# Kernel optimization log

Hardware: AMD Instinct MI355X
Metric: run time of the kernel (lower is better)

Reference implementation:

```python
import jax, jax.numpy as jnp
import numpy as np

N_NODES = 18870
HIDDEN = 256
K = 20
HEAD_HIDDEN = 512
N_CLASSES = 3
N_GENES_OUT = 6640
B = 1024
FALLBACK_SCALE = 1e-3
LN_EPS = 1e-5


def setup_inputs() -> dict:
    key = jax.random.key(0)
    ks = jax.random.split(key, 8)
    node_idx = jax.random.randint(ks[0], (B,), 0, N_NODES)
    topk_neighbors = jax.random.randint(ks[1], (N_NODES, K), 0, N_NODES)
    node_emb = jax.random.normal(ks[2], (N_NODES, HIDDEN), dtype=jnp.float32)
    fallback_emb = jax.random.normal(ks[3], (HIDDEN,), dtype=jnp.float32) * 0.02
    w_attn = jax.random.normal(ks[4], (HIDDEN,), dtype=jnp.float32) * 0.02
    ln_gamma = jnp.ones((2 * HIDDEN,), dtype=jnp.float32)
    ln_beta = jnp.zeros((2 * HIDDEN,), dtype=jnp.float32)
    W1 = jax.random.normal(ks[5], (2 * HIDDEN, HEAD_HIDDEN), dtype=jnp.float32) * 0.02
    b1 = jnp.zeros((HEAD_HIDDEN,), dtype=jnp.float32)
    W2 = jax.random.normal(ks[6], (HEAD_HIDDEN, N_CLASSES * N_GENES_OUT), dtype=jnp.float32) * 0.02
    b2 = jnp.zeros((N_CLASSES * N_GENES_OUT,), dtype=jnp.float32)
    return dict(node_idx=node_idx, topk_neighbors=topk_neighbors, node_emb=node_emb,
                fallback_emb=fallback_emb, w_attn=w_attn, ln_gamma=ln_gamma, ln_beta=ln_beta,
                W1=W1, b1=b1, W2=W2, b2=b2)


def reference(node_idx, topk_neighbors, node_emb, fallback_emb, w_attn,
              ln_gamma, ln_beta, W1, b1, W2, b2):
    valid = node_idx >= 0                                   # [B]
    safe_idx = jnp.where(valid, node_idx, 0)                # [B]
    graph_emb = node_emb[safe_idx]                          # [B, H]
    pert_emb = jnp.where(valid[:, None],
                         graph_emb + FALLBACK_SCALE * fallback_emb[None, :],
                         fallback_emb[None, :])              # [B, H]

    nbr_idx = topk_neighbors[safe_idx]                      # [B, K]
    valid_nbr = nbr_idx >= 0                                # [B, K]
    nbr_emb = node_emb[jnp.clip(nbr_idx, 0)]                # [B, K, H]
    nbr_emb = nbr_emb * valid_nbr[..., None].astype(nbr_emb.dtype)

    # Faithful to the original broadcast: scores[b,k] = pert_emb[b,0] * (nbr_emb[b,k] . w_attn)
    scores = pert_emb[:, 0:1] * jnp.einsum('bkh,h->bk', nbr_emb, w_attn)  # [B, K]
    scores = jnp.where(valid_nbr, scores, -1e9)
    has_valid = jnp.any(valid_nbr, axis=1, keepdims=True)   # [B, 1]
    attn = jnp.where(has_valid, jax.nn.softmax(scores, axis=-1),
                     jnp.zeros_like(scores))                # [B, K]
    context = jnp.einsum('bk,bkh->bh', attn, nbr_emb)       # [B, H]

    combined = jnp.concatenate([pert_emb, context], axis=-1)  # [B, 2H]
    mu = jnp.mean(combined, axis=-1, keepdims=True)
    var = jnp.mean(jnp.square(combined - mu), axis=-1, keepdims=True)
    x = (combined - mu) * jax.lax.rsqrt(var + LN_EPS) * ln_gamma + ln_beta
    h = jax.nn.gelu(x @ W1 + b1, approximate=False)          # [B, HH]
    logits = h @ W2 + b2                                     # [B, 3*6640]
    return logits.reshape(-1, N_CLASSES, N_GENES_OUT)


if __name__ == '__main__':
    out = reference(**setup_inputs())
    print(out.shape)
```

## Files before the change

kernel.cpp:

```cpp
#include <hip/hip_runtime.h>
#include <hip/hip_bf16.h>
#include <math.h>

#define HIDDEN 256
#define K_NBR 20
#define NB 1024

typedef __bf16 bf16x8 __attribute__((ext_vector_type(8)));
typedef float f32x4 __attribute__((ext_vector_type(4)));

__device__ __forceinline__ float wave_sum(float v) {
#pragma unroll
    for (int o = 32; o > 0; o >>= 1) v += __shfl_xor(v, o, 64);
    return v;
}

__device__ __forceinline__ void gload16(const void* g, void* l) {
    __builtin_amdgcn_global_load_lds(
        (const __attribute__((address_space(1))) void*)g,
        (__attribute__((address_space(3))) void*)l, 16, 0, 0);
}

__device__ __forceinline__ int swz_chunk(int g, int row) {
    return (g & ~7) | ((g & 7) ^ (row & 7));
}

__device__ __forceinline__ void attn_ln_body(
    int b, int t, const int* __restrict__ node_idx, const int* __restrict__ topk,
    const float* __restrict__ node_emb, const float* __restrict__ fallback,
    const float* __restrict__ w_attn, const float* __restrict__ gamma,
    const float* __restrict__ beta, __bf16* __restrict__ xb, int swz_on,
    float* pe, float (*nbr)[HIDDEN], int* nidx, float* sc, float* red)
{
    int lane = t & 63, w = t >> 6;

    int nid = node_idx[b];
    bool valid = nid >= 0;
    int safe = valid ? nid : 0;

    pe[t] = valid ? node_emb[(size_t)safe * HIDDEN + t] + 1e-3f * fallback[t]
                  : fallback[t];
    if (t < K_NBR) nidx[t] = topk[safe * K_NBR + t];
    __syncthreads();

    for (int r = 0; r < K_NBR; ++r) {
        int gi = nidx[r];
        nbr[r][t] = (gi >= 0) ? node_emb[(size_t)gi * HIDDEN + t] : 0.f;
    }
    __syncthreads();

    float pe0 = pe[0];
    float wa[4];
#pragma unroll
    for (int q = 0; q < 4; ++q) wa[q] = w_attn[lane + 64 * q];
    for (int k = w; k < K_NBR; k += 4) {
        float p = 0.f;
#pragma unroll
        for (int q = 0; q < 4; ++q) p += nbr[k][lane + 64 * q] * wa[q];
        p = wave_sum(p);
        if (lane == 0) sc[k] = (nidx[k] >= 0) ? pe0 * p : -1e9f;
    }
    __syncthreads();

    bool has_valid = false;
#pragma unroll
    for (int k = 0; k < K_NBR; ++k) has_valid |= (nidx[k] >= 0);
    float mx = -1e30f;
#pragma unroll
    for (int k = 0; k < K_NBR; ++k) mx = fmaxf(mx, sc[k]);
    float at[K_NBR];
    float s = 0.f;
#pragma unroll
    for (int k = 0; k < K_NBR; ++k) { at[k] = expf(sc[k] - mx); s += at[k]; }
    float inv = has_valid ? 1.f / s : 0.f;

    float ctx = 0.f;
#pragma unroll
    for (int k = 0; k < K_NBR; ++k) ctx += (at[k] * inv) * nbr[k][t];

    float v0 = pe[t], v1 = ctx;
    float s1 = wave_sum(v0 + v1);
    float s2 = wave_sum(v0 * v0 + v1 * v1);
    if (lane == 0) { red[w] = s1; red[4 + w] = s2; }
    __syncthreads();
    s1 = red[0] + red[1] + red[2] + red[3];
    s2 = red[4] + red[5] + red[6] + red[7];
    float mu = s1 / 512.f;
    float var = s2 / 512.f - mu * mu;
    float rs = rsqrtf(var + 1e-5f);

    size_t base = (size_t)b * 512;
    int mask = swz_on ? (b & 7) : 0;
    {
        int e = t;
        int g = e >> 3, off = e & 7;
        int gp = (g & ~7) | ((g & 7) ^ mask);
        xb[base + gp * 8 + off] = (__bf16)((v0 - mu) * rs * gamma[t] + beta[t]);
        e = 256 + t;
        g = e >> 3;
        gp = (g & ~7) | ((g & 7) ^ mask);
        xb[base + gp * 8 + off] = (__bf16)((v1 - mu) * rs * gamma[256 + t] + beta[256 + t]);
    }
}

__device__ __forceinline__ void transpose_body(
    const float* __restrict__ Wm, __bf16* __restrict__ WT,
    int Kd, int Nd, int Np, int bx, int by, int t)
{
    int n = bx * 64 + (t >> 2);
    int k0 = by * 32 + (t & 3) * 8;
    bool ok = n < Nd;
    bf16x8 v;
#pragma unroll
    for (int j = 0; j < 8; ++j) {
        float f = ok ? Wm[(size_t)(k0 + j) * Nd + n] : 0.f;
        v[j] = (__bf16)f;
    }
    if (n < Np) {
        int gp = swz_chunk(k0 >> 3, n);
        *(bf16x8*)(WT + (size_t)n * Kd + gp * 8) = v;
    }
}

__global__ __launch_bounds__(256) void prep_kernel(
    const int* __restrict__ node_idx, const int* __restrict__ topk,
    const float* __restrict__ node_emb, const float* __restrict__ fallback,
    const float* __restrict__ w_attn, const float* __restrict__ gamma,
    const float* __restrict__ beta, const float* __restrict__ W1,
    const float* __restrict__ W2, __bf16* __restrict__ xb,
    __bf16* __restrict__ w1t, __bf16* __restrict__ w2t)
{
    __shared__ float pe[HIDDEN];
    __shared__ float nbr[K_NBR][HIDDEN];
    __shared__ int   nidx[K_NBR];
    __shared__ float sc[K_NBR];
    __shared__ float red[8];

    int bid = blockIdx.x;
    int t = threadIdx.x;
    if (bid < 4992) {
        transpose_body(W2, w2t, 512, 19920, 19968, bid % 312, bid / 312, t);
        return;
    }
    bid -= 4992;
    if (bid < 128) {
        transpose_body(W1, w1t, 512, 512, 512, bid % 8, bid / 8, t);
        return;
    }
    bid -= 128;
    attn_ln_body(bid, t, node_idx, topk, node_emb, fallback, w_attn, gamma, beta,
                 xb, 1, pe, nbr, nidx, sc, red);
}

__global__ __launch_bounds__(256) void attn_ln_kernel(
    const int* __restrict__ node_idx, const int* __restrict__ topk,
    const float* __restrict__ node_emb, const float* __restrict__ fallback,
    const float* __restrict__ w_attn, const float* __restrict__ gamma,
    const float* __restrict__ beta, __bf16* __restrict__ xb, int swz_on)
{
    __shared__ float pe[HIDDEN];
    __shared__ float nbr[K_NBR][HIDDEN];
    __shared__ int   nidx[K_NBR];
    __shared__ float sc[K_NBR];
    __shared__ float red[8];
    attn_ln_body(blockIdx.x, threadIdx.x, node_idx, topk, node_emb, fallback,
                 w_attn, gamma, beta, xb, swz_on, pe, nbr, nidx, sc, red);
}

__global__ __launch_bounds__(256, 4) void gemm1_kernel(
    const __bf16* __restrict__ A, const __bf16* __restrict__ BT,
    const float* __restrict__ bias, __bf16* __restrict__ Cb,
    int M, int N, int K)
{
    constexpr int BK = 64;
    __shared__ __bf16 As[2][64 * BK];
    __shared__ __bf16 Bs[2][64 * BK];

    int t = threadIdx.x;
    int lane = t & 63;
    int wid = t >> 6;
    int wm = wid >> 1, wn = wid & 1;
    int lo = lane & 15, hi = lane >> 4;

    int nwg = gridDim.x;
    int bid = blockIdx.x;
    int cpx = nwg >> 3;
    int lid = (bid & 7) * cpx + (bid >> 3);
    int m0 = (lid & 15) * 64;
    int n0 = (lid >> 4) * 64;

    int rsub = lane >> 3, kc = lane & 7;

    auto STAGE = [&](int buf, int k0) {
#pragma unroll
        for (int j = 0; j < 2; ++j) {
            int rb = j * 32 + wid * 8;
            gload16(A + (size_t)(m0 + rb + rsub) * K + k0 + kc * 8, &As[buf][rb * BK]);
        }
#pragma unroll
        for (int j = 0; j < 2; ++j) {
            int rb = j * 32 + wid * 8;
            gload16(BT + (size_t)(n0 + rb + rsub) * K + k0 + kc * 8, &Bs[buf][rb * BK]);
        }
    };

    f32x4 acc[2][2];
#pragma unroll
    for (int m = 0; m < 2; ++m)
#pragma unroll
        for (int n = 0; n < 2; ++n)
            acc[m][n] = (f32x4){0.f, 0.f, 0.f, 0.f};

    auto COMPUTE = [&](int buf) {
#pragma unroll
        for (int ks = 0; ks < 2; ++ks) {
            bf16x8 af[2], bfr[2];
#pragma unroll
            for (int m = 0; m < 2; ++m) {
                int r = wm * 32 + m * 16 + lo;
                af[m] = *(const bf16x8*)&As[buf][r * BK + (((ks * 4 + hi) ^ (r & 7)) * 8)];
            }
#pragma unroll
            for (int n = 0; n < 2; ++n) {
                int r = wn * 32 + n * 16 + lo;
                bfr[n] = *(const bf16x8*)&Bs[buf][r * BK + (((ks * 4 + hi) ^ (r & 7)) * 8)];
            }
#pragma unroll
            for (int m = 0; m < 2; ++m)
#pragma unroll
                for (int n = 0; n < 2; ++n)
                    acc[m][n] = __builtin_amdgcn_mfma_f32_16x16x32_bf16(
                        af[m], bfr[n], acc[m][n], 0, 0, 0);
        }
    };

    const int nt = K / BK;
    STAGE(0, 0);
    for (int tt = 0; tt < nt - 1; ++tt) {
        STAGE((tt + 1) & 1, (tt + 1) * BK);
        asm volatile("s_waitcnt vmcnt(4)" ::: "memory");
        __builtin_amdgcn_s_barrier();
        __builtin_amdgcn_sched_barrier(0);
        COMPUTE(tt & 1);
        __builtin_amdgcn_sched_barrier(0);
        __builtin_amdgcn_s_barrier();
    }
    asm volatile("s_waitcnt vmcnt(0)" ::: "memory");
    __builtin_amdgcn_s_barrier();
    __builtin_amdgcn_sched_barrier(0);
    COMPUTE((nt - 1) & 1);

#pragma unroll
    for (int m = 0; m < 2; ++m) {
        int gr = m0 + wm * 32 + m * 16 + hi * 4;
#pragma unroll
        for (int n = 0; n < 2; ++n) {
            int gc = n0 + wn * 32 + n * 16 + lo;
            float bv = bias[gc];
#pragma unroll
            for (int r = 0; r < 4; ++r) {
                float v = acc[m][n][r] + bv;
                float g = v * 0.5f * (1.f + erff(v * 0.70710678118f));
                int row = gr + r;
                int gp = swz_chunk(gc >> 3, row);
                Cb[(size_t)row * N + gp * 8 + (gc & 7)] = (__bf16)g;
            }
        }
    }
}

__global__ __launch_bounds__(512, 4) void gemm2_kernel(
    const __bf16* __restrict__ A, const __bf16* __restrict__ BT,
    const float* __restrict__ bias, float* __restrict__ C,
    int M, int N, int K)
{
    constexpr int BK = 64;
    __shared__ __bf16 As[2][128 * BK];
    __shared__ __bf16 Bs[2][128 * BK];

    int t = threadIdx.x;
    int lane = t & 63;
    int wid = t >> 6;
    int wm = wid >> 2, wn = wid & 3;
    int lo = lane & 15, hi = lane >> 4;

    int nwg = gridDim.x;
    int bid = blockIdx.x;
    int cpx = nwg >> 3;
    int lid = (bid & 7) * cpx + (bid >> 3);
    int m0 = (lid & 7) * 128;
    int n0 = (lid >> 3) * 128;

    int rsub = lane >> 3, kc = lane & 7;

    auto STAGE = [&](int buf, int k0) {
#pragma unroll
        for (int j = 0; j < 2; ++j) {
            int rb = j * 64 + wid * 8;
            gload16(A + (size_t)(m0 + rb + rsub) * K + k0 + kc * 8, &As[buf][rb * BK]);
        }
#pragma unroll
        for (int j = 0; j < 2; ++j) {
            int rb = j * 64 + wid * 8;
            gload16(BT + (size_t)(n0 + rb + rsub) * K + k0 + kc * 8, &Bs[buf][rb * BK]);
        }
    };

    f32x4 acc[4][2];
#pragma unroll
    for (int m = 0; m < 4; ++m)
#pragma unroll
        for (int n = 0; n < 2; ++n)
            acc[m][n] = (f32x4){0.f, 0.f, 0.f, 0.f};

    auto COMPUTE = [&](int buf) {
#pragma unroll
        for (int ks = 0; ks < 2; ++ks) {
            bf16x8 af[4], bfr[2];
#pragma unroll
            for (int m = 0; m < 4; ++m) {
                int r = wm * 64 + m * 16 + lo;
                af[m] = *(const bf16x8*)&As[buf][r * BK + (((ks * 4 + hi) ^ (r & 7)) * 8)];
            }
#pragma unroll
            for (int n = 0; n < 2; ++n) {
                int r = wn * 32 + n * 16 + lo;
                bfr[n] = *(const bf16x8*)&Bs[buf][r * BK + (((ks * 4 + hi) ^ (r & 7)) * 8)];
            }
#pragma unroll
            for (int m = 0; m < 4; ++m)
#pragma unroll
                for (int n = 0; n < 2; ++n)
                    acc[m][n] = __builtin_amdgcn_mfma_f32_16x16x32_bf16(
                        af[m], bfr[n], acc[m][n], 0, 0, 0);
        }
    };

    const int nt = K / BK;
    STAGE(0, 0);
    for (int tt = 0; tt < nt - 1; ++tt) {
        STAGE((tt + 1) & 1, (tt + 1) * BK);
        asm volatile("s_waitcnt vmcnt(4)" ::: "memory");
        __builtin_amdgcn_s_barrier();
        __builtin_amdgcn_sched_barrier(0);
        COMPUTE(tt & 1);
        __builtin_amdgcn_sched_barrier(0);
        __builtin_amdgcn_s_barrier();
    }
    asm volatile("s_waitcnt vmcnt(0)" ::: "memory");
    __builtin_amdgcn_s_barrier();
    __builtin_amdgcn_sched_barrier(0);
    COMPUTE((nt - 1) & 1);

#pragma unroll
    for (int m = 0; m < 4; ++m) {
        int gr = m0 + wm * 64 + m * 16 + hi * 4;
#pragma unroll
        for (int n = 0; n < 2; ++n) {
            int gc = n0 + wn * 32 + n * 16 + lo;
            if (gc < N) {
                float bv = bias[gc];
#pragma unroll
                for (int r = 0; r < 4; ++r)
                    C[(size_t)(gr + r) * N + gc] = acc[m][n][r] + bv;
            }
        }
    }
}

template<bool GELU>
__global__ __launch_bounds__(256) void gemm_kernel(
    const __bf16* __restrict__ A, const float* __restrict__ Bm,
    const float* __restrict__ bias, float* __restrict__ Cf, __bf16* __restrict__ Cb,
    int M, int N, int K)
{
    constexpr int BK = 64;
    __shared__ bf16x8 As[2][128 * 8];
    __shared__ bf16x8 Bs[2][128 * 8];

    int t = threadIdx.x;
    int lane = t & 63;
    int wid = t >> 6;
    int wm = wid >> 1, wn = wid & 1;
    int lo = lane & 15, hi = lane >> 4;

    int n0 = blockIdx.x * 128;
    int m0 = blockIdx.y * 128;

    int cA = t & 7;
    int rA = t >> 3;
    int nl = t & 127;
    int kcb = t >> 7;

    bf16x8 a_st[4];
    bf16x8 b_st[4];

    auto LOAD = [&](int k0) {
#pragma unroll
        for (int i = 0; i < 4; ++i)
            a_st[i] = *(const bf16x8*)(A + (size_t)(m0 + rA + 32 * i) * K + k0 + cA * 8);
        int col = n0 + nl;
        bool ok = col < N;
#pragma unroll
        for (int i = 0; i < 4; ++i) {
            int kcv = kcb + 2 * i;
            bf16x8 v;
#pragma unroll
            for (int j = 0; j < 8; ++j) {
                float f = ok ? Bm[(size_t)(k0 + kcv * 8 + j) * N + col] : 0.f;
                v[j] = (__bf16)f;
            }
            b_st[i] = v;
        }
    };
    auto WRITE = [&](int buf) {
#pragma unroll
        for (int i = 0; i < 4; ++i) {
            int r = rA + 32 * i;
            As[buf][r * 8 + (cA ^ (r & 7))] = a_st[i];
        }
#pragma unroll
        for (int i = 0; i < 4; ++i) {
            int kcv = kcb + 2 * i;
            Bs[buf][nl * 8 + (kcv ^ (nl & 7))] = b_st[i];
        }
    };

    f32x4 acc[4][4];
#pragma unroll
    for (int m = 0; m < 4; ++m)
#pragma unroll
        for (int n = 0; n < 4; ++n)
            acc[m][n] = (f32x4){0.f, 0.f, 0.f, 0.f};

    auto COMPUTE = [&](int buf) {
#pragma unroll
        for (int ks = 0; ks < 2; ++ks) {
            bf16x8 af[4], bfr[4];
#pragma unroll
            for (int m = 0; m < 4; ++m) {
                int r = wm * 64 + m * 16 + lo;
                af[m] = As[buf][r * 8 + ((ks * 4 + hi) ^ (r & 7))];
            }
#pragma unroll
            for (int n = 0; n < 4; ++n) {
                int r = wn * 64 + n * 16 + lo;
                bfr[n] = Bs[buf][r * 8 + ((ks * 4 + hi) ^ (r & 7))];
            }
#pragma unroll
            for (int m = 0; m < 4; ++m)
#pragma unroll
                for (int n = 0; n < 4; ++n)
                    acc[m][n] = __builtin_amdgcn_mfma_f32_16x16x32_bf16(
                        af[m], bfr[n], acc[m][n], 0, 0, 0);
        }
    };

    const int nt = K / BK;
    LOAD(0);
    WRITE(0);
    __syncthreads();
    for (int tt = 0; tt < nt; ++tt) {
        int cur = tt & 1;
        if (tt + 1 < nt) LOAD((tt + 1) * BK);
        COMPUTE(cur);
        if (tt + 1 < nt) WRITE(cur ^ 1);
        __syncthreads();
    }

#pragma unroll
    for (int m = 0; m < 4; ++m) {
        int gr = m0 + wm * 64 + m * 16 + hi * 4;
#pragma unroll
        for (int n = 0; n < 4; ++n) {
            int gc = n0 + wn * 64 + n * 16 + lo;
            if (gc < N) {
                float bv = bias[gc];
#pragma unroll
                for (int r = 0; r < 4; ++r) {
                    float v = acc[m][n][r] + bv;
                    if constexpr (GELU) {
                        float g = v * 0.5f * (1.f + erff(v * 0.70710678118f));
                        Cb[(size_t)(gr + r) * N + gc] = (__bf16)g;
                    } else {
                        Cf[(size_t)(gr + r) * N + gc] = v;
                    }
                }
            }
        }
    }
}

extern "C" void kernel_launch(void* const* d_in, const int* in_sizes, int n_in,
                              void* d_out, int out_size, void* d_ws, size_t ws_size,
                              hipStream_t stream) {
    const int*   node_idx = (const int*)d_in[0];
    const int*   topk     = (const int*)d_in[1];
    const float* node_emb = (const float*)d_in[2];
    const float* fallback = (const float*)d_in[3];
    const float* w_attn   = (const float*)d_in[4];
    const float* gamma    = (const float*)d_in[5];
    const float* beta     = (const float*)d_in[6];
    const float* W1       = (const float*)d_in[7];
    const float* b1       = (const float*)d_in[8];
    const float* W2       = (const float*)d_in[9];
    const float* b2       = (const float*)d_in[10];
    float* out = (float*)d_out;

    const int M = 1024, Kd = 512, N1 = 512, N2 = 19920;
    const int N2p = 19968;

    __bf16* xb  = (__bf16*)d_ws;
    __bf16* h   = xb + (size_t)M * Kd;
    __bf16* w1t = h + (size_t)M * Kd;
    __bf16* w2t = w1t + (size_t)N1 * Kd;
    size_t needed = ((size_t)2 * M * Kd + (size_t)N1 * Kd + (size_t)N2p * Kd) * sizeof(__bf16);

    if (ws_size >= needed) {
        prep_kernel<<<4992 + 128 + 1024, 256, 0, stream>>>(
            node_idx, topk, node_emb, fallback, w_attn, gamma, beta, W1, W2,
            xb, w1t, w2t);

        gemm1_kernel<<<dim3(128), 256, 0, stream>>>(
            xb, w1t, b1, h, M, N1, Kd);

        gemm2_kernel<<<dim3(1248), 512, 0, stream>>>(
            h, w2t, b2, out, M, N2, Kd);
    } else {
        attn_ln_kernel<<<NB, 256, 0, stream>>>(node_idx, topk, node_emb, fallback,
                                               w_attn, gamma, beta, xb, 0);
        gemm_kernel<true><<<dim3(4, 8), 256, 0, stream>>>(
            xb, W1, b1, nullptr, h, M, N1, Kd);
        gemm_kernel<false><<<dim3(156, 8), 256, 0, stream>>>(
            h, W2, b2, out, nullptr, M, N2, Kd);
    }
}
```

Baseline: 74.73 us.

## Halve gemm2 K-tile to 32 with 2-bit swizzle and raise occupancy

The second GEMM's K-step drops from 64 to 32, so each thread stages one 16-byte load per operand per step. The LDS swizzle changes to a 2-bit XOR pattern on row>>1, applied consistently in the W2 transpose, the gemm1 output (h), and gemm2 reads. Launch bounds go to 8 blocks per CU, since the halved shared footprint is meant to allow more resident blocks and hide latency. The fallback path and the unused generic gemm are removed. The cost is twice as many barrier/wait iterations over K=512.

```diff
diff --git a/kernel.cpp b/kernel.cpp
--- a/kernel.cpp
+++ b/kernel.cpp
@@ -21,19 +21,21 @@
         (__attribute__((address_space(3))) void*)l, 16, 0, 0);
 }
 
-__device__ __forceinline__ int swz_chunk(int g, int row) {
+__device__ __forceinline__ int swz3(int g, int row) {
     return (g & ~7) | ((g & 7) ^ (row & 7));
+}
+__device__ __forceinline__ int swz2(int g, int row) {
+    return (g & ~3) | ((g & 3) ^ ((row >> 1) & 3));
 }
 
 __device__ __forceinline__ void attn_ln_body(
     int b, int t, const int* __restrict__ node_idx, const int* __restrict__ topk,
     const float* __restrict__ node_emb, const float* __restrict__ fallback,
     const float* __restrict__ w_attn, const float* __restrict__ gamma,
-    const float* __restrict__ beta, __bf16* __restrict__ xb, int swz_on,
+    const float* __restrict__ beta, __bf16* __restrict__ xb,
     float* pe, float (*nbr)[HIDDEN], int* nidx, float* sc, float* red)
 {
     int lane = t & 63, w = t >> 6;
-
     int nid = node_idx[b];
     bool valid = nid >= 0;
     int safe = valid ? nid : 0;
@@ -42,13 +44,11 @@
                   : fallback[t];
     if (t < K_NBR) nidx[t] = topk[safe * K_NBR + t];
     __syncthreads();
-
     for (int r = 0; r < K_NBR; ++r) {
         int gi = nidx[r];
         nbr[r][t] = (gi >= 0) ? node_emb[(size_t)gi * HIDDEN + t] : 0.f;
     }
     __syncthreads();
-
     float pe0 = pe[0];
     float wa[4];
 #pragma unroll
@@ -61,7 +61,6 @@
         if (lane == 0) sc[k] = (nidx[k] >= 0) ? pe0 * p : -1e9f;
     }
     __syncthreads();
-
     bool has_valid = false;
 #pragma unroll
     for (int k = 0; k < K_NBR; ++k) has_valid |= (nidx[k] >= 0);
@@ -73,11 +72,9 @@
 #pragma unroll
     for (int k = 0; k < K_NBR; ++k) { at[k] = expf(sc[k] - mx); s += at[k]; }
     float inv = has_valid ? 1.f / s : 0.f;
-
     float ctx = 0.f;
 #pragma unroll
     for (int k = 0; k < K_NBR; ++k) ctx += (at[k] * inv) * nbr[k][t];
-
     float v0 = pe[t], v1 = ctx;
     float s1 = wave_sum(v0 + v1);
     float s2 = wave_sum(v0 * v0 + v1 * v1);
@@ -88,9 +85,8 @@
     float mu = s1 / 512.f;
     float var = s2 / 512.f - mu * mu;
     float rs = rsqrtf(var + 1e-5f);
-
     size_t base = (size_t)b * 512;
-    int mask = swz_on ? (b & 7) : 0;
+    int mask = b & 7;
     {
         int e = t;
         int g = e >> 3, off = e & 7;
@@ -105,7 +101,7 @@
 
 __device__ __forceinline__ void transpose_body(
     const float* __restrict__ Wm, __bf16* __restrict__ WT,
-    int Kd, int Nd, int Np, int bx, int by, int t)
+    int Kd, int Nd, int Np, int bx, int by, int t, int two_bit)
 {
     int n = bx * 64 + (t >> 2);
     int k0 = by * 32 + (t & 3) * 8;
@@ -117,7 +113,8 @@
         v[j] = (__bf16)f;
     }
     if (n < Np) {
-        int gp = swz_chunk(k0 >> 3, n);
+        int g = k0 >> 3;
+        int gp = two_bit ? swz2(g, n) : swz3(g, n);
         *(bf16x8*)(WT + (size_t)n * Kd + gp * 8) = v;
     }
 }
@@ -135,36 +132,14 @@
     __shared__ int   nidx[K_NBR];
     __shared__ float sc[K_NBR];
     __shared__ float red[8];
-
     int bid = blockIdx.x;
     int t = threadIdx.x;
-    if (bid < 4992) {
-        transpose_body(W2, w2t, 512, 19920, 19968, bid % 312, bid / 312, t);
-        return;
-    }
+    if (bid < 4992) { transpose_body(W2, w2t, 512, 19920, 19968, bid % 312, bid / 312, t, 1); return; }
     bid -= 4992;
-    if (bid < 128) {
-        transpose_body(W1, w1t, 512, 512, 512, bid % 8, bid / 8, t);
-        return;
-    }
+    if (bid < 128) { transpose_body(W1, w1t, 512, 512, 512, bid % 8, bid / 8, t, 0); return; }
     bid -= 128;
     attn_ln_body(bid, t, node_idx, topk, node_emb, fallback, w_attn, gamma, beta,
-                 xb, 1, pe, nbr, nidx, sc, red);
-}
-
-__global__ __launch_bounds__(256) void attn_ln_kernel(
-    const int* __restrict__ node_idx, const int* __restrict__ topk,
-    const float* __restrict__ node_emb, const float* __restrict__ fallback,
-    const float* __restrict__ w_attn, const float* __restrict__ gamma,
-    const float* __restrict__ beta, __bf16* __restrict__ xb, int swz_on)
-{
-    __shared__ float pe[HIDDEN];
-    __shared__ float nbr[K_NBR][HIDDEN];
-    __shared__ int   nidx[K_NBR];
-    __shared__ float sc[K_NBR];
-    __shared__ float red[8];
-    attn_ln_body(blockIdx.x, threadIdx.x, node_idx, topk, node_emb, fallback,
-                 w_attn, gamma, beta, xb, swz_on, pe, nbr, nidx, sc, red);
+                 xb, pe, nbr, nidx, sc, red);
 }
 
 __global__ __launch_bounds__(256, 4) void gemm1_kernel(
@@ -208,8 +183,7 @@
 #pragma unroll
     for (int m = 0; m < 2; ++m)
 #pragma unroll
-        for (int n = 0; n < 2; ++n)
-            acc[m][n] = (f32x4){0.f, 0.f, 0.f, 0.f};
+        for (int n = 0; n < 2; ++n) acc[m][n] = (f32x4){0.f, 0.f, 0.f, 0.f};
 
     auto COMPUTE = [&](int buf) {
 #pragma unroll
@@ -262,19 +236,19 @@
                 float v = acc[m][n][r] + bv;
                 float g = v * 0.5f * (1.f + erff(v * 0.70710678118f));
                 int row = gr + r;
-                int gp = swz_chunk(gc >> 3, row);
+                int gp = swz2(gc >> 3, row);
                 Cb[(size_t)row * N + gp * 8 + (gc & 7)] = (__bf16)g;
             }
         }
     }
 }
 
-__global__ __launch_bounds__(512, 4) void gemm2_kernel(
+__global__ __launch_bounds__(512, 8) void gemm2_kernel(
     const __bf16* __restrict__ A, const __bf16* __restrict__ BT,
     const float* __restrict__ bias, float* __restrict__ C,
     int M, int N, int K)
 {
-    constexpr int BK = 64;
+    constexpr int BK = 32;
     __shared__ __bf16 As[2][128 * BK];
     __shared__ __bf16 Bs[2][128 * BK];
 
@@ -291,56 +265,46 @@
     int m0 = (lid & 7) * 128;
     int n0 = (lid >> 3) * 128;
 
-    int rsub = lane >> 3, kc = lane & 7;
-
-    auto STAGE = [&](int buf, int k0) {
-#pragma unroll
-        for (int j = 0; j < 2; ++j) {
-            int rb = j * 64 + wid * 8;
-            gload16(A + (size_t)(m0 + rb + rsub) * K + k0 + kc * 8, &As[buf][rb * BK]);
-        }
-#pragma unroll
-        for (int j = 0; j < 2; ++j) {
-            int rb = j * 64 + wid * 8;
-            gload16(BT + (size_t)(n0 + rb + rsub) * K + k0 + kc * 8, &Bs[buf][rb * BK]);
-        }
+    int srow = t >> 2;
+    int ssl = t & 3;
+
+    auto STAGE = [&](int buf, int tt) {
+        int k0 = tt * BK;
+        gload16(A + (size_t)(m0 + srow) * K + k0 + ssl * 8, &As[buf][wid * 512]);
+        gload16(BT + (size_t)(n0 + srow) * K + k0 + ssl * 8, &Bs[buf][wid * 512]);
     };
 
     f32x4 acc[4][2];
 #pragma unroll
     for (int m = 0; m < 4; ++m)
 #pragma unroll
-        for (int n = 0; n < 2; ++n)
-            acc[m][n] = (f32x4){0.f, 0.f, 0.f, 0.f};
+        for (int n = 0; n < 2; ++n) acc[m][n] = (f32x4){0.f, 0.f, 0.f, 0.f};
 
     auto COMPUTE = [&](int buf) {
-#pragma unroll
-        for (int ks = 0; ks < 2; ++ks) {
-            bf16x8 af[4], bfr[2];
-#pragma unroll
-            for (int m = 0; m < 4; ++m) {
-                int r = wm * 64 + m * 16 + lo;
-                af[m] = *(const bf16x8*)&As[buf][r * BK + (((ks * 4 + hi) ^ (r & 7)) * 8)];
-            }
-#pragma unroll
-            for (int n = 0; n < 2; ++n) {
-                int r = wn * 32 + n * 16 + lo;
-                bfr[n] = *(const bf16x8*)&Bs[buf][r * BK + (((ks * 4 + hi) ^ (r & 7)) * 8)];
-            }
-#pragma unroll
-            for (int m = 0; m < 4; ++m)
-#pragma unroll
-                for (int n = 0; n < 2; ++n)
-                    acc[m][n] = __builtin_amdgcn_mfma_f32_16x16x32_bf16(
-                        af[m], bfr[n], acc[m][n], 0, 0, 0);
-        }
+        bf16x8 af[4], bfr[2];
+#pragma unroll
+        for (int m = 0; m < 4; ++m) {
+            int r = wm * 64 + m * 16 + lo;
+            af[m] = *(const bf16x8*)&As[buf][r * BK + ((hi ^ ((r >> 1) & 3)) * 8)];
+        }
+#pragma unroll
+        for (int n = 0; n < 2; ++n) {
+            int r = wn * 32 + n * 16 + lo;
+            bfr[n] = *(const bf16x8*)&Bs[buf][r * BK + ((hi ^ ((r >> 1) & 3)) * 8)];
+        }
+#pragma unroll
+        for (int m = 0; m < 4; ++m)
+#pragma unroll
+            for (int n = 0; n < 2; ++n)
+                acc[m][n] = __builtin_amdgcn_mfma_f32_16x16x32_bf16(
+                    af[m], bfr[n], acc[m][n], 0, 0, 0);
     };
 
     const int nt = K / BK;
     STAGE(0, 0);
     for (int tt = 0; tt < nt - 1; ++tt) {
-        STAGE((tt + 1) & 1, (tt + 1) * BK);
-        asm volatile("s_waitcnt vmcnt(4)" ::: "memory");
+        STAGE((tt + 1) & 1, tt + 1);
+        asm volatile("s_waitcnt vmcnt(2)" ::: "memory");
         __builtin_amdgcn_s_barrier();
         __builtin_amdgcn_sched_barrier(0);
         COMPUTE(tt & 1);
@@ -363,129 +327,6 @@
 #pragma unroll
                 for (int r = 0; r < 4; ++r)
                     C[(size_t)(gr + r) * N + gc] = acc[m][n][r] + bv;
-            }
-        }
-    }
-}
-
-template<bool GELU>
-__global__ __launch_bounds__(256) void gemm_kernel(
-    const __bf16* __restrict__ A, const float* __restrict__ Bm,
-    const float* __restrict__ bias, float* __restrict__ Cf, __bf16* __restrict__ Cb,
-    int M, int N, int K)
-{
-    constexpr int BK = 64;
-    __shared__ bf16x8 As[2][128 * 8];
-    __shared__ bf16x8 Bs[2][128 * 8];
-
-    int t = threadIdx.x;
-    int lane = t & 63;
-    int wid = t >> 6;
-    int wm = wid >> 1, wn = wid & 1;
-    int lo = lane & 15, hi = lane >> 4;
-
-    int n0 = blockIdx.x * 128;
-    int m0 = blockIdx.y * 128;
-
-    int cA = t & 7;
-    int rA = t >> 3;
-    int nl = t & 127;
-    int kcb = t >> 7;
-
-    bf16x8 a_st[4];
-    bf16x8 b_st[4];
-
-    auto LOAD = [&](int k0) {
-#pragma unroll
-        for (int i = 0; i < 4; ++i)
-            a_st[i] = *(const bf16x8*)(A + (size_t)(m0 + rA + 32 * i) * K + k0 + cA * 8);
-        int col = n0 + nl;
-        bool ok = col < N;
-#pragma unroll
-        for (int i = 0; i < 4; ++i) {
-            int kcv = kcb + 2 * i;
-            bf16x8 v;
-#pragma unroll
-            for (int j = 0; j < 8; ++j) {
-                float f = ok ? Bm[(size_t)(k0 + kcv * 8 + j) * N + col] : 0.f;
-                v[j] = (__bf16)f;
-            }
-            b_st[i] = v;
-        }
-    };
-    auto WRITE = [&](int buf) {
-#pragma unroll
-        for (int i = 0; i < 4; ++i) {
-            int r = rA + 32 * i;
-            As[buf][r * 8 + (cA ^ (r & 7))] = a_st[i];
-        }
-#pragma unroll
-        for (int i = 0; i < 4; ++i) {
-            int kcv = kcb + 2 * i;
-            Bs[buf][nl * 8 + (kcv ^ (nl & 7))] = b_st[i];
-        }
-    };
-
-    f32x4 acc[4][4];
-#pragma unroll
-    for (int m = 0; m < 4; ++m)
-#pragma unroll
-        for (int n = 0; n < 4; ++n)
-            acc[m][n] = (f32x4){0.f, 0.f, 0.f, 0.f};
-
-    auto COMPUTE = [&](int buf) {
-#pragma unroll
-        for (int ks = 0; ks < 2; ++ks) {
-            bf16x8 af[4], bfr[4];
-#pragma unroll
-            for (int m = 0; m < 4; ++m) {
-                int r = wm * 64 + m * 16 + lo;
-                af[m] = As[buf][r * 8 + ((ks * 4 + hi) ^ (r & 7))];
-            }
-#pragma unroll
-            for (int n = 0; n < 4; ++n) {
-                int r = wn * 64 + n * 16 + lo;
-                bfr[n] = Bs[buf][r * 8 + ((ks * 4 + hi) ^ (r & 7))];
-            }
-#pragma unroll
-            for (int m = 0; m < 4; ++m)
-#pragma unroll
-                for (int n = 0; n < 4; ++n)
-                    acc[m][n] = __builtin_amdgcn_mfma_f32_16x16x32_bf16(
-                        af[m], bfr[n], acc[m][n], 0, 0, 0);
-        }
-    };
-
-    const int nt = K / BK;
-    LOAD(0);
-    WRITE(0);
-    __syncthreads();
-    for (int tt = 0; tt < nt; ++tt) {
-        int cur = tt & 1;
-        if (tt + 1 < nt) LOAD((tt + 1) * BK);
-        COMPUTE(cur);
-        if (tt + 1 < nt) WRITE(cur ^ 1);
-        __syncthreads();
-    }
-
-#pragma unroll
-    for (int m = 0; m < 4; ++m) {
-        int gr = m0 + wm * 64 + m * 16 + hi * 4;
-#pragma unroll
-        for (int n = 0; n < 4; ++n) {
-            int gc = n0 + wn * 64 + n * 16 + lo;
-            if (gc < N) {
-                float bv = bias[gc];
-#pragma unroll
-                for (int r = 0; r < 4; ++r) {
-                    float v = acc[m][n][r] + bv;
-                    if constexpr (GELU) {
-                        float g = v * 0.5f * (1.f + erff(v * 0.70710678118f));
-                        Cb[(size_t)(gr + r) * N + gc] = (__bf16)g;
-                    } else {
-                        Cf[(size_t)(gr + r) * N + gc] = v;
-                    }
-                }
             }
         }
     }
@@ -514,24 +355,15 @@
     __bf16* h   = xb + (size_t)M * Kd;
     __bf16* w1t = h + (size_t)M * Kd;
     __bf16* w2t = w1t + (size_t)N1 * Kd;
-    size_t needed = ((size_t)2 * M * Kd + (size_t)N1 * Kd + (size_t)N2p * Kd) * sizeof(__bf16);
-
-    if (ws_size >= needed) {
-        prep_kernel<<<4992 + 128 + 1024, 256, 0, stream>>>(
-            node_idx, topk, node_emb, fallback, w_attn, gamma, beta, W1, W2,
-            xb, w1t, w2t);
-
-        gemm1_kernel<<<dim3(128), 256, 0, stream>>>(
-            xb, w1t, b1, h, M, N1, Kd);
-
-        gemm2_kernel<<<dim3(1248), 512, 0, stream>>>(
-            h, w2t, b2, out, M, N2, Kd);
-    } else {
-        attn_ln_kernel<<<NB, 256, 0, stream>>>(node_idx, topk, node_emb, fallback,
-                                               w_attn, gamma, beta, xb, 0);
-        gemm_kernel<true><<<dim3(4, 8), 256, 0, stream>>>(
-            xb, W1, b1, nullptr, h, M, N1, Kd);
-        gemm_kernel<false><<<dim3(156, 8), 256, 0, stream>>>(
-            h, W2, b2, out, nullptr, M, N2, Kd);
-    }
-}
+
+    prep_kernel<<<4992 + 128 + 1024, 256, 0, stream>>>(
+        node_idx, topk, node_emb, fallback, w_attn, gamma, beta, W1, W2,
+        xb, w1t, w2t);
+
+    gemm1_kernel<<<dim3(128), 256, 0, stream>>>(
+        xb, w1t, b1, h, M, N1, Kd);
+
+    gemm2_kernel<<<dim3(1248), 512, 0, stream>>>(
+        h, w2t, b2, out, M, N2, Kd);
+    (void)ws_size;
+}
```

Result: no change. 75.25 us (+0.7%).
